# Kernel optimization log

Measured on AMD Instinct MI355X. Metric: run time of the kernel, lower is better.

## Reference

```python
import jax, jax.numpy as jnp
import numpy as np

K = 3
HEADS = 6
EMBED = 192
KD = EMBED // HEADS  # 32
SCALE = float(KD) ** -0.5


def setup_inputs() -> dict:
    key = jax.random.key(0)
    ks = jax.random.split(key, 5)
    B, H, W, C = 8, 252, 192, 64
    x = jax.random.normal(ks[0], (B, H, W, C), dtype=jnp.float32)
    v_w = jax.random.normal(ks[1], (C, EMBED), dtype=jnp.float32) * (C ** -0.5)
    attn_w = jax.random.normal(ks[2], (C, K ** 4 * HEADS), dtype=jnp.float32) * (C ** -0.5)
    attn_b = jnp.zeros((K ** 4 * HEADS,), dtype=jnp.float32)
    out_w = jax.random.normal(ks[3], (EMBED, EMBED), dtype=jnp.float32) * (EMBED ** -0.5)
    out_b = jnp.zeros((EMBED,), dtype=jnp.float32)
    return {"x": x, "v_w": v_w, "attn_w": attn_w, "attn_b": attn_b,
            "out_w": out_w, "out_b": out_b}


def reference(x, v_w, attn_w, attn_b, out_w, out_b):
    B, H, W, C = x.shape
    hh, ww = -(-H // K), -(-W // K)          # ceil division
    ph, pw = hh * K - H, ww * K - W          # bottom/right zero padding
    xp = jnp.pad(x, ((0, 0), (0, ph), (0, pw), (0, 0))) if (ph or pw) else x

    # value branch: unfold into k*k windows -> [B, hh, ww, heads, k^2, kd]
    v = xp @ v_w
    v = v.reshape(B, hh, K, ww, K, HEADS, KD)
    v = v.transpose(0, 1, 3, 5, 2, 4, 6).reshape(B, hh, ww, HEADS, K * K, KD)

    # attention branch: k x k average pool (stride k) then dense to k^4*heads
    pooled = xp.reshape(B, hh, K, ww, K, C).mean(axis=(2, 4))  # [B, hh, ww, C]
    attn = (pooled @ attn_w + attn_b) * SCALE
    attn = attn.reshape(B, hh, ww, HEADS, K * K, K * K)
    attn = jax.nn.softmax(attn, axis=-1)

    # windowed attention: [.., k^2, k^2] @ [.., k^2, kd]
    out = attn @ v                                             # [B, hh, ww, heads, k^2, kd]

    # fold back to spatial layout, drop padding
    out = out.reshape(B, hh, ww, HEADS, K, K, KD)
    out = out.transpose(0, 1, 4, 2, 5, 3, 6).reshape(B, hh * K, ww * K, EMBED)
    out = out[:, :H, :W, :]
    return out @ out_w + out_b
```

## Files before the change

kernel.cpp:

```cpp
#include <hip/hip_runtime.h>
#include <hip/hip_bf16.h>

#define NB   8
#define NH   252
#define NW   192
#define NC   64
#define HHD  84
#define WWD  64
#define NE   192
#define NO   486
#define NWIN (NB*HHD*WWD)
#define NM   (NWIN*9)
#define SCALE_F 0.17677669529663687f

typedef __bf16 bf16x8 __attribute__((ext_vector_type(8)));
typedef float floatx4 __attribute__((ext_vector_type(4)));

__device__ __attribute__((aligned(16))) __hip_bfloat16 g_owT[NE * NE];
__device__ __attribute__((aligned(16))) __hip_bfloat16 g_vwT[NE * NC];

__device__ __forceinline__ float bfu2f(__bf16 v) { return (float)v; }

__global__ __launch_bounds__(256) void kt_transpose(
    const float* __restrict__ ow, const float* __restrict__ vw)
{
    int t = blockIdx.x * 256 + threadIdx.x;
    if (t < 36864) {
        int n = t / 192;
        int k = t - n * 192;
        g_owT[n * 192 + k] = __float2bfloat16(ow[k * 192 + n]);
    } else {
        int tt = t - 36864;
        int n = tt / 64;
        int k = tt - n * 64;
        g_vwT[n * 64 + k] = __float2bfloat16(vw[k * 192 + n]);
    }
}

__global__ __launch_bounds__(256) void ka_window(
    const float* __restrict__ x,
    const float* __restrict__ attn_w,
    const float* __restrict__ attn_b,
    __hip_bfloat16* __restrict__ out_pre)
{
    __shared__ __attribute__((aligned(16))) __bf16 xw[80 * 72];
    __shared__ __attribute__((aligned(16))) __bf16 vS[80 * 200];
    __shared__ float pooled[8][64];
    __shared__ float attnS[8][488];

    const int tid = threadIdx.x;
    const int lane = tid & 63;
    const int wv = tid >> 6;
    const int m16 = lane & 15;
    const int quad = lane >> 4;
    const int wbase = blockIdx.x * 8;

    #pragma unroll
    for (int it = 0; it < 18; ++it) {
        int t = it * 256 + tid;
        int row = t >> 6;
        int c = t & 63;
        int win = row / 9;
        int q = row - win * 9;
        int widx = wbase + win;
        int b = widx / 5376;
        int rem = widx - b * 5376;
        int i = rem >> 6;
        int j = rem & 63;
        int pr = q / 3;
        int pc = q - pr * 3;
        float xv = x[((b * NH + (i * 3 + pr)) * NW + (j * 3 + pc)) * NC + c];
        xw[row * 72 + c] = (__bf16)xv;
    }
    __syncthreads();

    #pragma unroll
    for (int it = 0; it < 2; ++it) {
        int t = it * 256 + tid;
        int win = t >> 6;
        int c = t & 63;
        float s = 0.f;
        #pragma unroll
        for (int q = 0; q < 9; ++q) s += bfu2f(xw[(win * 9 + q) * 72 + c]);
        pooled[win][c] = s * (1.f / 9.f);
    }
    __syncthreads();

    {
        float a0[8], a1[8];
        #pragma unroll
        for (int g = 0; g < 8; ++g) { a0[g] = 0.f; a1[g] = 0.f; }
        const int o0 = tid;
        const int o1 = tid + 256;
        const bool has1 = (o1 < NO);
        for (int c = 0; c < 64; ++c) {
            float w0 = attn_w[c * NO + o0];
            float w1 = has1 ? attn_w[c * NO + o1] : 0.f;
            #pragma unroll
            for (int g = 0; g < 8; ++g) {
                float p = pooled[g][c];
                a0[g] = fmaf(p, w0, a0[g]);
                a1[g] = fmaf(p, w1, a1[g]);
            }
        }
        float b0 = attn_b[o0];
        #pragma unroll
        for (int g = 0; g < 8; ++g) attnS[g][o0] = (a0[g] + b0) * SCALE_F;
        if (has1) {
            float b1 = attn_b[o1];
            #pragma unroll
            for (int g = 0; g < 8; ++g) attnS[g][o1] = (a1[g] + b1) * SCALE_F;
        }
    }
    __syncthreads();

    #pragma unroll
    for (int it = 0; it < 2; ++it) {
        int t = it * 256 + tid;
        if (t < 432) {
            int win = t / 54;
            int g = t - win * 54;
            float* a = &attnS[win][g * 9];
            float m = a[0];
            #pragma unroll
            for (int q = 1; q < 9; ++q) m = fmaxf(m, a[q]);
            float e[9];
            float s = 0.f;
            #pragma unroll
            for (int q = 0; q < 9; ++q) { e[q] = __expf(a[q] - m); s += e[q]; }
            float inv = 1.f / s;
            #pragma unroll
            for (int q = 0; q < 9; ++q) a[q] = e[q] * inv;
        }
    }
    __syncthreads();

    {
        const __bf16* Bv = (const __bf16*)g_vwT;
        bf16x8 bfragV[2][3];
        #pragma unroll
        for (int ks = 0; ks < 2; ++ks)
            #pragma unroll
            for (int nt = 0; nt < 3; ++nt)
                bfragV[ks][nt] = *(const bf16x8*)(Bv + (wv * 48 + nt * 16 + m16) * 64 + ks * 32 + quad * 8);

        floatx4 acc[5][3];
        #pragma unroll
        for (int mt = 0; mt < 5; ++mt)
            #pragma unroll
            for (int nt = 0; nt < 3; ++nt) {
                acc[mt][nt][0] = 0.f; acc[mt][nt][1] = 0.f;
                acc[mt][nt][2] = 0.f; acc[mt][nt][3] = 0.f;
            }
        #pragma unroll
        for (int ks = 0; ks < 2; ++ks)
            #pragma unroll
            for (int mt = 0; mt < 5; ++mt) {
                bf16x8 afrag = *(const bf16x8*)(&xw[(mt * 16 + m16) * 72 + ks * 32 + quad * 8]);
                #pragma unroll
                for (int nt = 0; nt < 3; ++nt)
                    acc[mt][nt] = __builtin_amdgcn_mfma_f32_16x16x32_bf16(afrag, bfragV[ks][nt], acc[mt][nt], 0, 0, 0);
            }
        #pragma unroll
        for (int mt = 0; mt < 5; ++mt)
            #pragma unroll
            for (int nt = 0; nt < 3; ++nt)
                #pragma unroll
                for (int r = 0; r < 4; ++r) {
                    int row = mt * 16 + quad * 4 + r;
                    int col = wv * 48 + nt * 16 + m16;
                    vS[row * 200 + col] = (__bf16)acc[mt][nt][r];
                }
    }
    __syncthreads();

    #pragma unroll
    for (int pass = 0; pass < 2; ++pass) {
        int t = pass * 256 + tid;
        if (t < 384) {
            int win = t / 48;
            int e0 = t - win * 48;
            float v0[9], v1[9], v2[9], v3[9];
            #pragma unroll
            for (int q = 0; q < 9; ++q) {
                const __bf16* vr = &vS[(win * 9 + q) * 200];
                v0[q] = bfu2f(vr[e0]);
                v1[q] = bfu2f(vr[e0 + 48]);
                v2[q] = bfu2f(vr[e0 + 96]);
                v3[q] = bfu2f(vr[e0 + 144]);
            }
            int widx = wbase + win;
            int b = widx / 5376;
            int rem = widx - b * 5376;
            int i = rem >> 6;
            int j = rem & 63;
            const float* at = &attnS[win][0];
            const int h0 = (e0) >> 5;
            const int h1 = (e0 + 48) >> 5;
            const int h2 = (e0 + 96) >> 5;
            const int h3 = (e0 + 144) >> 5;
            #pragma unroll
            for (int p = 0; p < 9; ++p) {
                const float* r0 = at + h0 * 81 + p * 9;
                const float* r1 = at + h1 * 81 + p * 9;
                const float* r2 = at + h2 * 81 + p * 9;
                const float* r3 = at + h3 * 81 + p * 9;
                float o0 = 0.f, o1 = 0.f, o2 = 0.f, o3 = 0.f;
                #pragma unroll
                for (int q = 0; q < 9; ++q) {
                    o0 = fmaf(r0[q], v0[q], o0);
                    o1 = fmaf(r1[q], v1[q], o1);
                    o2 = fmaf(r2[q], v2[q], o2);
                    o3 = fmaf(r3[q], v3[q], o3);
                }
                int pr = p / 3;
                int pc = p - pr * 3;
                int base = ((b * NH + (i * 3 + pr)) * NW + (j * 3 + pc)) * NE;
                out_pre[base + e0]       = __float2bfloat16(o0);
                out_pre[base + e0 + 48]  = __float2bfloat16(o1);
                out_pre[base + e0 + 96]  = __float2bfloat16(o2);
                out_pre[base + e0 + 144] = __float2bfloat16(o3);
            }
        }
    }
}

__global__ __launch_bounds__(256) void kb_gemm(
    const __hip_bfloat16* __restrict__ Ain,
    const float* __restrict__ out_b,
    float* __restrict__ out)
{
    __shared__ __attribute__((aligned(16))) ushort As[64 * 200];

    const int tid = threadIdx.x;
    const int lane = tid & 63;
    const int wv = tid >> 6;
    const int m16 = lane & 15;
    const int quad = lane >> 4;

    float bias[3];
    #pragma unroll
    for (int nt = 0; nt < 3; ++nt) bias[nt] = out_b[wv * 48 + nt * 16 + m16];

    const __bf16* Bu = (const __bf16*)g_owT;
    bf16x8 bfragB[6][3];
    #pragma unroll
    for (int ks = 0; ks < 6; ++ks)
        #pragma unroll
        for (int nt = 0; nt < 3; ++nt)
            bfragB[ks][nt] = *(const bf16x8*)(Bu + (wv * 48 + nt * 16 + m16) * 192 + ks * 32 + quad * 8);

    const ushort* Au = (const ushort*)Ain;

    for (int tI = 0; tI < 8; ++tI) {
        int mbase = (blockIdx.x * 8 + tI) * 64;
        __syncthreads();
        #pragma unroll
        for (int it = 0; it < 6; ++it) {
            int chunk = it * 256 + tid;
            int r = chunk / 24;
            int pos = chunk - r * 24;
            uint4 vdat = *(const uint4*)(Au + (mbase + r) * 192 + pos * 8);
            *(uint4*)(&As[r * 200 + pos * 8]) = vdat;
        }
        __syncthreads();

        floatx4 acc[4][3];
        #pragma unroll
        for (int mt = 0; mt < 4; ++mt)
            #pragma unroll
            for (int nt = 0; nt < 3; ++nt) {
                acc[mt][nt][0] = 0.f; acc[mt][nt][1] = 0.f;
                acc[mt][nt][2] = 0.f; acc[mt][nt][3] = 0.f;
            }

        #pragma unroll
        for (int ks = 0; ks < 6; ++ks)
            #pragma unroll
            for (int mt = 0; mt < 4; ++mt) {
                bf16x8 afrag = *(const bf16x8*)(&As[(mt * 16 + m16) * 200 + ks * 32 + quad * 8]);
                #pragma unroll
                for (int nt = 0; nt < 3; ++nt)
                    acc[mt][nt] = __builtin_amdgcn_mfma_f32_16x16x32_bf16(afrag, bfragB[ks][nt], acc[mt][nt], 0, 0, 0);
            }

        #pragma unroll
        for (int mt = 0; mt < 4; ++mt)
            #pragma unroll
            for (int nt = 0; nt < 3; ++nt)
                #pragma unroll
                for (int r = 0; r < 4; ++r) {
                    int row = mbase + mt * 16 + quad * 4 + r;
                    int col = wv * 48 + nt * 16 + m16;
                    out[row * NE + col] = acc[mt][nt][r] + bias[nt];
                }
    }
}

extern "C" void kernel_launch(void* const* d_in, const int* in_sizes, int n_in,
                              void* d_out, int out_size, void* d_ws, size_t ws_size,
                              hipStream_t stream)
{
    const float* x      = (const float*)d_in[0];
    const float* v_w    = (const float*)d_in[1];
    const float* attn_w = (const float*)d_in[2];
    const float* attn_b = (const float*)d_in[3];
    const float* out_w  = (const float*)d_in[4];
    const float* out_b  = (const float*)d_in[5];
    float* out = (float*)d_out;

    __hip_bfloat16* out_pre = (__hip_bfloat16*)d_ws;

    hipLaunchKernelGGL(kt_transpose, dim3(192), dim3(256), 0, stream, out_w, v_w);
    hipLaunchKernelGGL(ka_window, dim3(NWIN / 8), dim3(256), 0, stream,
                       x, attn_w, attn_b, out_pre);
    hipLaunchKernelGGL(kb_gemm, dim3(NM / 64 / 8), dim3(256), 0, stream,
                       out_pre, out_b, out);
}
```

Before: 581.1 us.

## Fuse window attention with output projection via precombined per-head value-output weights

Folds v_w and out_w into a per-head combined weight W_h = v_w[:,h] @ out_w[h,:] in a prep kernel, so each window computes attn_h @ x (block-diagonal MFMA) followed by x_h @ W_h accumulated directly into the final output. This removes the bf16 intermediate round-trip to global memory and the separate GEMM kernel. The attention-logit dense layer also moves to MFMA using a transposed bf16 attn_w. In exchange there are more MFMA FLOPs per window (six heads times a K=64 projection), a per-head loop with two barriers, and attention probabilities stored in bf16.

```diff
diff --git a/kernel.cpp b/kernel.cpp
--- a/kernel.cpp
+++ b/kernel.cpp
@@ -10,106 +10,125 @@
 #define NE   192
 #define NO   486
 #define NWIN (NB*HHD*WWD)
-#define NM   (NWIN*9)
 #define SCALE_F 0.17677669529663687f
 
 typedef __bf16 bf16x8 __attribute__((ext_vector_type(8)));
 typedef float floatx4 __attribute__((ext_vector_type(4)));
 
-__device__ __attribute__((aligned(16))) __hip_bfloat16 g_owT[NE * NE];
-__device__ __attribute__((aligned(16))) __hip_bfloat16 g_vwT[NE * NC];
-
-__device__ __forceinline__ float bfu2f(__bf16 v) { return (float)v; }
-
-__global__ __launch_bounds__(256) void kt_transpose(
-    const float* __restrict__ ow, const float* __restrict__ vw)
+__device__ __attribute__((aligned(16))) __hip_bfloat16 g_WT[NE * 384];
+__device__ __attribute__((aligned(16))) __hip_bfloat16 g_awT[NO * 64];
+
+__device__ __forceinline__ bf16x8 bf16x8_zero() {
+    bf16x8 z;
+    #pragma unroll
+    for (int j = 0; j < 8; ++j) z[j] = (__bf16)0.f;
+    return z;
+}
+
+__global__ __launch_bounds__(256) void kt_prep(
+    const float* __restrict__ vw, const float* __restrict__ ow,
+    const float* __restrict__ aw)
 {
     int t = blockIdx.x * 256 + threadIdx.x;
-    if (t < 36864) {
-        int n = t / 192;
-        int k = t - n * 192;
-        g_owT[n * 192 + k] = __float2bfloat16(ow[k * 192 + n]);
+    if (t < NE * 384) {
+        int e  = t / 384;
+        int hc = t - e * 384;
+        int h  = hc >> 6;
+        int c  = hc & 63;
+        float s = 0.f;
+        #pragma unroll
+        for (int d = 0; d < 32; ++d)
+            s = fmaf(vw[c * NE + h * 32 + d], ow[(h * 32 + d) * NE + e], s);
+        g_WT[e * 384 + hc] = __float2bfloat16(s);
     } else {
-        int tt = t - 36864;
-        int n = tt / 64;
-        int k = tt - n * 64;
-        g_vwT[n * 64 + k] = __float2bfloat16(vw[k * 192 + n]);
-    }
-}
-
-__global__ __launch_bounds__(256) void ka_window(
+        int tt = t - NE * 384;
+        if (tt < NO * 64) {
+            int n = tt >> 6;
+            int c = tt & 63;
+            g_awT[tt] = __float2bfloat16(aw[c * NO + n]);
+        }
+    }
+}
+
+__global__ __launch_bounds__(256, 3) void ka_fused(
     const float* __restrict__ x,
-    const float* __restrict__ attn_w,
     const float* __restrict__ attn_b,
-    __hip_bfloat16* __restrict__ out_pre)
+    const float* __restrict__ out_b,
+    float* __restrict__ out)
 {
-    __shared__ __attribute__((aligned(16))) __bf16 xw[80 * 72];
-    __shared__ __attribute__((aligned(16))) __bf16 vS[80 * 200];
-    __shared__ float pooled[8][64];
-    __shared__ float attnS[8][488];
-
-    const int tid = threadIdx.x;
+    __shared__ __attribute__((aligned(16))) __bf16 xwT[64 * 104];
+    __shared__ __attribute__((aligned(16))) __bf16 pooledB[8 * 64];
+    __shared__ __attribute__((aligned(16))) __bf16 attnS[8 * 486];
+    __shared__ __attribute__((aligned(16))) __bf16 attnBD[80 * 104];
+    __shared__ __attribute__((aligned(16))) __bf16 Ph[80 * 72];
+
+    const int tid  = threadIdx.x;
     const int lane = tid & 63;
-    const int wv = tid >> 6;
-    const int m16 = lane & 15;
+    const int wv   = tid >> 6;
+    const int m16  = lane & 15;
     const int quad = lane >> 4;
     const int wbase = blockIdx.x * 8;
 
+    const int bB   = wbase / 5376;
+    const int remB = wbase - bB * 5376;
+    const int iB   = remB >> 6;
+    const int jB   = remB & 63;
+    const int xbase = ((bB * NH + iB * 3) * NW + jB * 3) * NC;
+
     #pragma unroll
     for (int it = 0; it < 18; ++it) {
-        int t = it * 256 + tid;
-        int row = t >> 6;
-        int c = t & 63;
+        int row = it * 4 + wv;
         int win = row / 9;
-        int q = row - win * 9;
-        int widx = wbase + win;
-        int b = widx / 5376;
-        int rem = widx - b * 5376;
-        int i = rem >> 6;
-        int j = rem & 63;
-        int pr = q / 3;
-        int pc = q - pr * 3;
-        float xv = x[((b * NH + (i * 3 + pr)) * NW + (j * 3 + pc)) * NC + c];
-        xw[row * 72 + c] = (__bf16)xv;
+        int q   = row - win * 9;
+        int pr  = q / 3;
+        int pc  = q - pr * 3;
+        float xv = x[xbase + (pr * NW + win * 3 + pc) * NC + lane];
+        xwT[lane * 104 + row] = (__bf16)xv;
+    }
+    {
+        int rr = tid >> 2, ss = tid & 3;
+        *(uint4*)(&xwT[rr * 104 + 72 + ss * 8]) = make_uint4(0u, 0u, 0u, 0u);
+    }
+    #pragma unroll
+    for (int it = 0; it < 5; ++it) {
+        int ch = it * 256 + tid;
+        if (ch < 1040) *(uint4*)(&attnBD[ch * 8]) = make_uint4(0u, 0u, 0u, 0u);
     }
     __syncthreads();
 
     #pragma unroll
     for (int it = 0; it < 2; ++it) {
-        int t = it * 256 + tid;
-        int win = t >> 6;
-        int c = t & 63;
+        int win = it * 4 + wv;
         float s = 0.f;
         #pragma unroll
-        for (int q = 0; q < 9; ++q) s += bfu2f(xw[(win * 9 + q) * 72 + c]);
-        pooled[win][c] = s * (1.f / 9.f);
+        for (int q = 0; q < 9; ++q) s += (float)xwT[lane * 104 + win * 9 + q];
+        pooledB[win * 64 + lane] = (__bf16)(s * (1.f / 9.f));
     }
     __syncthreads();
 
     {
-        float a0[8], a1[8];
-        #pragma unroll
-        for (int g = 0; g < 8; ++g) { a0[g] = 0.f; a1[g] = 0.f; }
-        const int o0 = tid;
-        const int o1 = tid + 256;
-        const bool has1 = (o1 < NO);
-        for (int c = 0; c < 64; ++c) {
-            float w0 = attn_w[c * NO + o0];
-            float w1 = has1 ? attn_w[c * NO + o1] : 0.f;
-            #pragma unroll
-            for (int g = 0; g < 8; ++g) {
-                float p = pooled[g][c];
-                a0[g] = fmaf(p, w0, a0[g]);
-                a1[g] = fmaf(p, w1, a1[g]);
-            }
-        }
-        float b0 = attn_b[o0];
-        #pragma unroll
-        for (int g = 0; g < 8; ++g) attnS[g][o0] = (a0[g] + b0) * SCALE_F;
-        if (has1) {
-            float b1 = attn_b[o1];
-            #pragma unroll
-            for (int g = 0; g < 8; ++g) attnS[g][o1] = (a1[g] + b1) * SCALE_F;
+        bf16x8 afragP[2];
+        #pragma unroll
+        for (int ks = 0; ks < 2; ++ks)
+            afragP[ks] = *(const bf16x8*)(&pooledB[m16 * 64 + ks * 32 + quad * 8]);
+        const __bf16* Aw = (const __bf16*)g_awT;
+        #pragma unroll
+        for (int i = 0; i < 8; ++i) {
+            int tile = wv * 8 + i;
+            int n = tile * 16 + m16;
+            bool nvalid = (tile < 31) && (n < NO);
+            bf16x8 b0 = nvalid ? *(const bf16x8*)(Aw + n * 64 + quad * 8)      : bf16x8_zero();
+            bf16x8 b1 = nvalid ? *(const bf16x8*)(Aw + n * 64 + 32 + quad * 8) : bf16x8_zero();
+            floatx4 acc;
+            acc[0] = 0.f; acc[1] = 0.f; acc[2] = 0.f; acc[3] = 0.f;
+            acc = __builtin_amdgcn_mfma_f32_16x16x32_bf16(afragP[0], b0, acc, 0, 0, 0);
+            acc = __builtin_amdgcn_mfma_f32_16x16x32_bf16(afragP[1], b1, acc, 0, 0, 0);
+            if (nvalid && quad < 2) {
+                float bn = attn_b[n];
+                #pragma unroll
+                for (int r = 0; r < 4; ++r)
+                    attnS[(quad * 4 + r) * NO + n] = (__bf16)((acc[r] + bn) * SCALE_F);
+            }
         }
     }
     __syncthreads();
@@ -120,181 +139,110 @@
         if (t < 432) {
             int win = t / 54;
             int g = t - win * 54;
-            float* a = &attnS[win][g * 9];
-            float m = a[0];
-            #pragma unroll
-            for (int q = 1; q < 9; ++q) m = fmaxf(m, a[q]);
-            float e[9];
+            __bf16* a = &attnS[win * NO + g * 9];
+            float v[9];
+            v[0] = (float)a[0];
+            float m = v[0];
+            #pragma unroll
+            for (int q = 1; q < 9; ++q) { v[q] = (float)a[q]; m = fmaxf(m, v[q]); }
             float s = 0.f;
             #pragma unroll
-            for (int q = 0; q < 9; ++q) { e[q] = __expf(a[q] - m); s += e[q]; }
+            for (int q = 0; q < 9; ++q) { v[q] = __expf(v[q] - m); s += v[q]; }
             float inv = 1.f / s;
             #pragma unroll
-            for (int q = 0; q < 9; ++q) a[q] = e[q] * inv;
-        }
-    }
-    __syncthreads();
-
-    {
-        const __bf16* Bv = (const __bf16*)g_vwT;
-        bf16x8 bfragV[2][3];
-        #pragma unroll
-        for (int ks = 0; ks < 2; ++ks)
+            for (int q = 0; q < 9; ++q) a[q] = (__bf16)(v[q] * inv);
+        }
+    }
+    __syncthreads();
+
+    bf16x8 bfragX[3];
+    #pragma unroll
+    for (int ks = 0; ks < 3; ++ks)
+        bfragX[ks] = *(const bf16x8*)(&xwT[(wv * 16 + m16) * 104 + ks * 32 + quad * 8]);
+
+    float bias[3];
+    #pragma unroll
+    for (int nt = 0; nt < 3; ++nt) bias[nt] = out_b[wv * 48 + nt * 16 + m16];
+
+    floatx4 accF[5][3];
+    #pragma unroll
+    for (int mt = 0; mt < 5; ++mt)
+        #pragma unroll
+        for (int nt = 0; nt < 3; ++nt) {
+            accF[mt][nt][0] = 0.f; accF[mt][nt][1] = 0.f;
+            accF[mt][nt][2] = 0.f; accF[mt][nt][3] = 0.f;
+        }
+
+    const __bf16* Wt = (const __bf16*)g_WT;
+
+    for (int h = 0; h < 6; ++h) {
+        #pragma unroll
+        for (int it = 0; it < 3; ++it) {
+            int t = it * 256 + tid;
+            if (t < 648) {
+                int win = t / 81;
+                int r81 = t - win * 81;
+                int p = r81 / 9;
+                int q = r81 - p * 9;
+                attnBD[(win * 9 + p) * 104 + win * 9 + q] = attnS[win * NO + h * 81 + r81];
+            }
+        }
+        __syncthreads();
+
+        {
+            floatx4 accP[5];
+            #pragma unroll
+            for (int mt = 0; mt < 5; ++mt) {
+                accP[mt][0] = 0.f; accP[mt][1] = 0.f; accP[mt][2] = 0.f; accP[mt][3] = 0.f;
+            }
+            #pragma unroll
+            for (int ks = 0; ks < 3; ++ks)
+                #pragma unroll
+                for (int mt = 0; mt < 5; ++mt) {
+                    bf16x8 af = *(const bf16x8*)(&attnBD[(mt * 16 + m16) * 104 + ks * 32 + quad * 8]);
+                    accP[mt] = __builtin_amdgcn_mfma_f32_16x16x32_bf16(af, bfragX[ks], accP[mt], 0, 0, 0);
+                }
+            #pragma unroll
+            for (int mt = 0; mt < 5; ++mt)
+                #pragma unroll
+                for (int r = 0; r < 4; ++r)
+                    Ph[(mt * 16 + quad * 4 + r) * 72 + wv * 16 + m16] = (__bf16)accP[mt][r];
+        }
+        __syncthreads();
+
+        #pragma unroll
+        for (int ks = 0; ks < 2; ++ks) {
+            bf16x8 bw[3];
             #pragma unroll
             for (int nt = 0; nt < 3; ++nt)
-                bfragV[ks][nt] = *(const bf16x8*)(Bv + (wv * 48 + nt * 16 + m16) * 64 + ks * 32 + quad * 8);
-
-        floatx4 acc[5][3];
-        #pragma unroll
-        for (int mt = 0; mt < 5; ++mt)
-            #pragma unroll
-            for (int nt = 0; nt < 3; ++nt) {
-                acc[mt][nt][0] = 0.f; acc[mt][nt][1] = 0.f;
-                acc[mt][nt][2] = 0.f; acc[mt][nt][3] = 0.f;
-            }
-        #pragma unroll
-        for (int ks = 0; ks < 2; ++ks)
+                bw[nt] = *(const bf16x8*)(Wt + (wv * 48 + nt * 16 + m16) * 384 + h * 64 + ks * 32 + quad * 8);
             #pragma unroll
             for (int mt = 0; mt < 5; ++mt) {
-                bf16x8 afrag = *(const bf16x8*)(&xw[(mt * 16 + m16) * 72 + ks * 32 + quad * 8]);
+                bf16x8 af = *(const bf16x8*)(&Ph[(mt * 16 + m16) * 72 + ks * 32 + quad * 8]);
                 #pragma unroll
                 for (int nt = 0; nt < 3; ++nt)
-                    acc[mt][nt] = __builtin_amdgcn_mfma_f32_16x16x32_bf16(afrag, bfragV[ks][nt], acc[mt][nt], 0, 0, 0);
-            }
-        #pragma unroll
-        for (int mt = 0; mt < 5; ++mt)
-            #pragma unroll
-            for (int nt = 0; nt < 3; ++nt)
-                #pragma unroll
-                for (int r = 0; r < 4; ++r) {
-                    int row = mt * 16 + quad * 4 + r;
-                    int col = wv * 48 + nt * 16 + m16;
-                    vS[row * 200 + col] = (__bf16)acc[mt][nt][r];
-                }
-    }
-    __syncthreads();
-
-    #pragma unroll
-    for (int pass = 0; pass < 2; ++pass) {
-        int t = pass * 256 + tid;
-        if (t < 384) {
-            int win = t / 48;
-            int e0 = t - win * 48;
-            float v0[9], v1[9], v2[9], v3[9];
-            #pragma unroll
-            for (int q = 0; q < 9; ++q) {
-                const __bf16* vr = &vS[(win * 9 + q) * 200];
-                v0[q] = bfu2f(vr[e0]);
-                v1[q] = bfu2f(vr[e0 + 48]);
-                v2[q] = bfu2f(vr[e0 + 96]);
-                v3[q] = bfu2f(vr[e0 + 144]);
-            }
-            int widx = wbase + win;
-            int b = widx / 5376;
-            int rem = widx - b * 5376;
-            int i = rem >> 6;
-            int j = rem & 63;
-            const float* at = &attnS[win][0];
-            const int h0 = (e0) >> 5;
-            const int h1 = (e0 + 48) >> 5;
-            const int h2 = (e0 + 96) >> 5;
-            const int h3 = (e0 + 144) >> 5;
-            #pragma unroll
-            for (int p = 0; p < 9; ++p) {
-                const float* r0 = at + h0 * 81 + p * 9;
-                const float* r1 = at + h1 * 81 + p * 9;
-                const float* r2 = at + h2 * 81 + p * 9;
-                const float* r3 = at + h3 * 81 + p * 9;
-                float o0 = 0.f, o1 = 0.f, o2 = 0.f, o3 = 0.f;
-                #pragma unroll
-                for (int q = 0; q < 9; ++q) {
-                    o0 = fmaf(r0[q], v0[q], o0);
-                    o1 = fmaf(r1[q], v1[q], o1);
-                    o2 = fmaf(r2[q], v2[q], o2);
-                    o3 = fmaf(r3[q], v3[q], o3);
-                }
+                    accF[mt][nt] = __builtin_amdgcn_mfma_f32_16x16x32_bf16(af, bw[nt], accF[mt][nt], 0, 0, 0);
+            }
+        }
+    }
+
+    const int obase = ((bB * NH + iB * 3) * NW + jB * 3) * NE;
+    #pragma unroll
+    for (int mt = 0; mt < 5; ++mt)
+        #pragma unroll
+        for (int r = 0; r < 4; ++r) {
+            int row = mt * 16 + quad * 4 + r;
+            if (row < 72) {
+                int win = row / 9;
+                int p = row - win * 9;
                 int pr = p / 3;
                 int pc = p - pr * 3;
-                int base = ((b * NH + (i * 3 + pr)) * NW + (j * 3 + pc)) * NE;
-                out_pre[base + e0]       = __float2bfloat16(o0);
-                out_pre[base + e0 + 48]  = __float2bfloat16(o1);
-                out_pre[base + e0 + 96]  = __float2bfloat16(o2);
-                out_pre[base + e0 + 144] = __float2bfloat16(o3);
-            }
-        }
-    }
-}
-
-__global__ __launch_bounds__(256) void kb_gemm(
-    const __hip_bfloat16* __restrict__ Ain,
-    const float* __restrict__ out_b,
-    float* __restrict__ out)
-{
-    __shared__ __attribute__((aligned(16))) ushort As[64 * 200];
-
-    const int tid = threadIdx.x;
-    const int lane = tid & 63;
-    const int wv = tid >> 6;
-    const int m16 = lane & 15;
-    const int quad = lane >> 4;
-
-    float bias[3];
-    #pragma unroll
-    for (int nt = 0; nt < 3; ++nt) bias[nt] = out_b[wv * 48 + nt * 16 + m16];
-
-    const __bf16* Bu = (const __bf16*)g_owT;
-    bf16x8 bfragB[6][3];
-    #pragma unroll
-    for (int ks = 0; ks < 6; ++ks)
-        #pragma unroll
-        for (int nt = 0; nt < 3; ++nt)
-            bfragB[ks][nt] = *(const bf16x8*)(Bu + (wv * 48 + nt * 16 + m16) * 192 + ks * 32 + quad * 8);
-
-    const ushort* Au = (const ushort*)Ain;
-
-    for (int tI = 0; tI < 8; ++tI) {
-        int mbase = (blockIdx.x * 8 + tI) * 64;
-        __syncthreads();
-        #pragma unroll
-        for (int it = 0; it < 6; ++it) {
-            int chunk = it * 256 + tid;
-            int r = chunk / 24;
-            int pos = chunk - r * 24;
-            uint4 vdat = *(const uint4*)(Au + (mbase + r) * 192 + pos * 8);
-            *(uint4*)(&As[r * 200 + pos * 8]) = vdat;
-        }
-        __syncthreads();
-
-        floatx4 acc[4][3];
-        #pragma unroll
-        for (int mt = 0; mt < 4; ++mt)
-            #pragma unroll
-            for (int nt = 0; nt < 3; ++nt) {
-                acc[mt][nt][0] = 0.f; acc[mt][nt][1] = 0.f;
-                acc[mt][nt][2] = 0.f; acc[mt][nt][3] = 0.f;
-            }
-
-        #pragma unroll
-        for (int ks = 0; ks < 6; ++ks)
-            #pragma unroll
-            for (int mt = 0; mt < 4; ++mt) {
-                bf16x8 afrag = *(const bf16x8*)(&As[(mt * 16 + m16) * 200 + ks * 32 + quad * 8]);
+                int base = obase + (pr * NW + win * 3 + pc) * NE;
                 #pragma unroll
                 for (int nt = 0; nt < 3; ++nt)
-                    acc[mt][nt] = __builtin_amdgcn_mfma_f32_16x16x32_bf16(afrag, bfragB[ks][nt], acc[mt][nt], 0, 0, 0);
-            }
-
-        #pragma unroll
-        for (int mt = 0; mt < 4; ++mt)
-            #pragma unroll
-            for (int nt = 0; nt < 3; ++nt)
-                #pragma unroll
-                for (int r = 0; r < 4; ++r) {
-                    int row = mbase + mt * 16 + quad * 4 + r;
-                    int col = wv * 48 + nt * 16 + m16;
-                    out[row * NE + col] = acc[mt][nt][r] + bias[nt];
-                }
-    }
+                    out[base + wv * 48 + nt * 16 + m16] = accF[mt][nt][r] + bias[nt];
+            }
+        }
 }
 
 extern "C" void kernel_launch(void* const* d_in, const int* in_sizes, int n_in,
@@ -308,12 +256,9 @@
     const float* out_w  = (const float*)d_in[4];
     const float* out_b  = (const float*)d_in[5];
     float* out = (float*)d_out;
-
-    __hip_bfloat16* out_pre = (__hip_bfloat16*)d_ws;
-
-    hipLaunchKernelGGL(kt_transpose, dim3(192), dim3(256), 0, stream, out_w, v_w);
-    hipLaunchKernelGGL(ka_window, dim3(NWIN / 8), dim3(256), 0, stream,
-                       x, attn_w, attn_b, out_pre);
-    hipLaunchKernelGGL(kb_gemm, dim3(NM / 64 / 8), dim3(256), 0, stream,
-                       out_pre, out_b, out);
-}
+    (void)d_ws; (void)ws_size; (void)in_sizes; (void)n_in; (void)out_size;
+
+    hipLaunchKernelGGL(kt_prep, dim3(410), dim3(256), 0, stream, v_w, out_w, attn_w);
+    hipLaunchKernelGGL(ka_fused, dim3(NWIN / 8), dim3(256), 0, stream,
+                       x, attn_b, out_b, out);
+}
```

New measurement: 494.6 us. 14.9% less time.
